# Kernel tuning notes

Measured on AMD Instinct MI355X. Metric: run time of the kernel, lower is better.

Reference implementation:

```python
import jax, jax.numpy as jnp
import numpy as np

B, T, C, H, E, MIN_E = 4, 2048, 1024, 128, 16, 2
IS_CAUSAL = False


def setup_inputs() -> dict:
    key = jax.random.key(0)
    ks = jax.random.split(key, 6)
    lim_qkv = float(np.sqrt(6.0 / (C + H)))
    inp = {
        "hidden_states": jax.random.normal(ks[0], (B, T, C), jnp.float32),
        "sim_matrix": jax.random.normal(ks[1], (C, E), jnp.float32),
        "gates": jnp.zeros((E,), jnp.float32),
        "q_proj": jax.random.uniform(ks[2], (E, C, H), jnp.float32, -lim_qkv, lim_qkv),
        "k_proj": jax.random.uniform(ks[3], (E, C, H), jnp.float32, -lim_qkv, lim_qkv),
        "v_proj": jax.random.uniform(ks[4], (E, C, H), jnp.float32, -lim_qkv, lim_qkv),
        "o_proj": jax.random.uniform(ks[5], (E, H, C), jnp.float32, -lim_qkv, lim_qkv),
    }
    return inp


def _forward(hidden_states, sim_matrix, gates, q_proj, k_proj, v_proj, o_proj):
    b, t, c = hidden_states.shape
    n = b * t
    x = hidden_states.reshape(n, c)

    # ---- gating (faithful to _gating_logic) ----
    xn = x / jnp.maximum(jnp.linalg.norm(x, axis=-1, keepdims=True), 1e-12)
    sn = sim_matrix / jnp.maximum(jnp.linalg.norm(sim_matrix, axis=0, keepdims=True), 1e-12)
    logits = xn @ sn - jax.nn.sigmoid(gates)          # [n, E]
    gated = jax.nn.relu(logits)
    # STE: forward = (gated > 0), backward = identity
    hard = (gated > 0).astype(gated.dtype)
    mask = gated + jax.lax.stop_gradient(hard - gated)
    inactive = (jnp.sum(hard, axis=1) == 0)
    # fallback: top-MIN_E logits for tokens with no active expert
    _, fb_idx = jax.lax.top_k(logits, MIN_E)
    fb = jnp.zeros((n, logits.shape[1]), gated.dtype).at[
        jnp.arange(n)[:, None], fb_idx].set(1.0)
    put = jax.lax.stop_gradient(inactive[:, None].astype(gated.dtype) * fb)
    mask = mask * (1.0 - put) + put                   # index_put semantics
    masked = jnp.where(mask > 0, gated, -jnp.inf)
    w = jax.nn.softmax(masked, axis=-1)               # routing weights [n, E]

    # ---- MoE dispatch/combine (dense-equivalent: w is exactly 0 where mask==0) ----
    def moe_proj(p):  # p: [E, C, H] -> [n, H]
        y = jnp.einsum('nc,ech->neh', x, p)
        return jnp.einsum('ne,neh->nh', w, y)

    q = moe_proj(q_proj).reshape(b, t, -1)
    k = moe_proj(k_proj).reshape(b, t, -1)
    v = moe_proj(v_proj).reshape(b, t, -1)

    # single-head SDPA, default scale 1/sqrt(head_dim)
    h = q.shape[-1]
    scores = jnp.einsum('bth,bsh->bts', q, k) / jnp.sqrt(jnp.asarray(h, q.dtype))
    if IS_CAUSAL and t > 1:
        causal = jnp.tril(jnp.ones((t, t), bool))
        scores = jnp.where(causal[None], scores, -jnp.inf)
    attn = jax.nn.softmax(scores, axis=-1)
    o = jnp.einsum('bts,bsh->bth', attn, v).reshape(n, h)

    # output MoE combine
    z = jnp.einsum('ne,nh->enh', w, o)                # [E, n, H]
    out = jnp.einsum('enh,ehc->nc', z, o_proj)
    return out.reshape(b, t, c)


def reference(hidden_states, sim_matrix, gates, q_proj, k_proj, v_proj, o_proj):
    return _forward(hidden_states, sim_matrix, gates, q_proj, k_proj, v_proj, o_proj)
```

## Files before the change

kernel.cpp:

```cpp
#include <hip/hip_runtime.h>
#include <hip/hip_bf16.h>
#include <math.h>

#define NBATCH 4
#define NT     2048
#define NC     1024
#define NH     128
#define NE     16
#define NTOK   (NBATCH * NT)
#define CAP    18432
#define NT2_MAX 152

typedef __bf16 bf16x8 __attribute__((ext_vector_type(8)));
typedef __bf16 bf16x4 __attribute__((ext_vector_type(4)));
typedef float  f32x4  __attribute__((ext_vector_type(4)));

__device__ __forceinline__ __bf16 f2bf(float f) { return (__bf16)f; }

#define BARRIER() __builtin_amdgcn_s_barrier()
#define SFENCE()  __builtin_amdgcn_sched_barrier(0)
#define VMWAIT(n) asm volatile("s_waitcnt vmcnt(" #n ")" ::: "memory")
#define LGKMWAIT0() asm volatile("s_waitcnt lgkmcnt(0)" ::: "memory")

__device__ __forceinline__ void gl_lds16(const void* g, void* l) {
  __builtin_amdgcn_global_load_lds((const __attribute__((address_space(1))) void*)g,
                                   (__attribute__((address_space(3))) void*)l, 16, 0, 0);
}

__device__ __forceinline__ const __bf16* swz_src(const __bf16* row0, size_t stride,
                                                 int tid, int i) {
  int lin = (tid + 256 * i) * 16;
  int r = lin >> 7, cb = lin & 127;
  return row0 + (size_t)r * stride + ((cb ^ ((r & 7) << 4)) >> 1);
}

__global__ void k_transpose_all(const float* __restrict__ qp, const float* __restrict__ kp,
                                const float* __restrict__ vp, const float* __restrict__ op,
                                __bf16* __restrict__ pqt, __bf16* __restrict__ pkt,
                                __bf16* __restrict__ pvt, __bf16* __restrict__ pot,
                                const float* __restrict__ sim, const float* __restrict__ gates,
                                double* __restrict__ snorm, double* __restrict__ sig,
                                int* __restrict__ ctrl) {
  __shared__ float tile[32][33];
  __shared__ double red[16][17];
  int z = blockIdx.y;
  int tid = threadIdx.x;
  if (z == 64) {
    if (blockIdx.x != 0) return;
    if (tid < 128) ctrl[tid] = 0;
    int e = tid & 15, chunk = tid >> 4;
    double a = 0.0;
#pragma unroll 4
    for (int j = 0; j < 64; j++) {
      double v = (double)sim[(chunk * 64 + j) * NE + e];
      a += v * v;
    }
    red[chunk][e] = a;
    __syncthreads();
    if (tid < 16) {
      double s = 0.0;
      for (int k = 0; k < 16; k++) s += red[k][tid];
      snorm[tid] = fmax(sqrt(s), 1e-12);
      sig[tid] = 1.0 / (1.0 + exp(-(double)gates[tid]));
    }
    return;
  }
  const float* in;
  __bf16* out;
  int R, Cd, g, r0, c0;
  if (z < 48) {
    int which = z >> 4; g = z & 15; R = 1024; Cd = 128;
    in = which == 0 ? qp : (which == 1 ? kp : vp);
    out = which == 0 ? pqt : (which == 1 ? pkt : pvt);
    r0 = (blockIdx.x >> 2) * 32; c0 = (blockIdx.x & 3) * 32;
  } else {
    g = z - 48; R = 128; Cd = 1024;
    in = op; out = pot;
    r0 = (blockIdx.x & 3) * 32; c0 = (blockIdx.x >> 2) * 32;
  }
  int tx = tid & 31, ty0 = tid >> 5;
  const float* src = in + (size_t)g * R * Cd;
  __bf16* dst = out + (size_t)g * R * Cd;
#pragma unroll
  for (int ty = ty0; ty < 32; ty += 8)
    tile[ty][tx] = src[(size_t)(r0 + ty) * Cd + (c0 + tx)];
  __syncthreads();
#pragma unroll
  for (int ty = ty0; ty < 32; ty += 8)
    dst[(size_t)(c0 + ty) * R + (r0 + tx)] = f2bf(tile[tx][ty]);
}

__global__ __launch_bounds__(256, 2) void k_gating3(const float* __restrict__ x,
                                                    const float* __restrict__ sim,
                                                    const double* __restrict__ snorm,
                                                    const double* __restrict__ sig,
                                                    float* __restrict__ w_all,
                                                    int* __restrict__ counts,
                                                    __bf16* __restrict__ xbf) {
  __shared__ union {
    struct {
      float xs_[16][66];
      float ss_[16][66];
    } s;
    double red[8][32][2][17];
  } u;
  __shared__ float w_lds[16][16];
  __shared__ int cnt_lds[16];
  int tid = threadIdx.x;
  if (tid < 16) cnt_lds[tid] = 0;
  int cg = tid & 31, tkg = tid >> 5;
  int tok0 = blockIdx.x * 16;

  double acc[2][17];
#pragma unroll
  for (int t = 0; t < 2; t++)
#pragma unroll
    for (int i = 0; i < 17; i++) acc[t][i] = 0.0;

  int xr0 = tid >> 4, xc4 = (tid & 15) * 4;
  int sr = tid >> 2, se4 = (tid & 3) * 4;

  float4 xa, sv;
  auto ldchunk = [&](int c0) {
    xa = *(const float4*)(x + (size_t)(tok0 + xr0) * NC + c0 + xc4);
    sv = *(const float4*)(sim + (size_t)(c0 + sr) * NE + se4);
  };
  auto stchunk = [&]() {
    *(float4*)&u.s.xs_[xr0][xc4] = xa;
    u.s.ss_[se4 + 0][sr] = sv.x;
    u.s.ss_[se4 + 1][sr] = sv.y;
    u.s.ss_[se4 + 2][sr] = sv.z;
    u.s.ss_[se4 + 3][sr] = sv.w;
  };
  auto stxbf = [&](int c0) {
    bf16x4 a;
    a[0]=f2bf(xa.x); a[1]=f2bf(xa.y); a[2]=f2bf(xa.z); a[3]=f2bf(xa.w);
    *(bf16x4*)(xbf + (size_t)(tok0 + xr0) * NC + c0 + xc4) = a;
  };

  ldchunk(0);
  for (int ch = 0; ch < 16; ch++) {
    stchunk();
    stxbf(ch * 64);
    __syncthreads();
    if (ch < 15) ldchunk((ch + 1) * 64);
    double xd[2][2];
#pragma unroll
    for (int t = 0; t < 2; t++) {
      float2 xv = *(const float2*)&u.s.xs_[tkg * 2 + t][cg * 2];
      xd[t][0] = (double)xv.x;
      xd[t][1] = (double)xv.y;
      acc[t][16] += xd[t][0] * xd[t][0] + xd[t][1] * xd[t][1];
    }
#pragma unroll
    for (int e = 0; e < 16; e++) {
      float2 sv2 = *(const float2*)&u.s.ss_[e][cg * 2];
      double s0 = (double)sv2.x, s1 = (double)sv2.y;
#pragma unroll
      for (int t = 0; t < 2; t++)
        acc[t][e] += xd[t][0] * s0 + xd[t][1] * s1;
    }
    __syncthreads();
  }

#pragma unroll
  for (int t = 0; t < 2; t++)
#pragma unroll
    for (int i = 0; i < 17; i++)
      u.red[tkg][cg][t][i] = acc[t][i];
  __syncthreads();

  if (tid < 16) {
    double dots[17];
    for (int i = 0; i < 17; i++) {
      double s = 0.0;
      for (int c = 0; c < 32; c++) s += u.red[tid >> 1][c][tid & 1][i];
      dots[i] = s;
    }
    double xn = fmax(sqrt(dots[16]), 1e-12);
    double logits[NE];
    unsigned act = 0;
    int cnt = 0;
    for (int ee = 0; ee < NE; ee++) {
      logits[ee] = dots[ee] / (xn * snorm[ee]) - sig[ee];
      if (logits[ee] > 0.0) { act |= 1u << ee; cnt++; }
    }
    if (cnt == 0) {
      int i1 = 0; double b1 = logits[0];
      for (int ee = 1; ee < NE; ee++) if (logits[ee] > b1) { b1 = logits[ee]; i1 = ee; }
      int i2 = -1; double b2 = -1e300;
      for (int ee = 0; ee < NE; ee++) if (ee != i1 && logits[ee] > b2) { b2 = logits[ee]; i2 = ee; }
      act = (1u << i1) | (1u << i2);
    }
    double m = -1e300;
    for (int ee = 0; ee < NE; ee++) if ((act >> ee) & 1) m = fmax(m, fmax(logits[ee], 0.0));
    double s = 0.0, wvv[NE];
    for (int ee = 0; ee < NE; ee++) {
      if ((act >> ee) & 1) { wvv[ee] = exp(fmax(logits[ee], 0.0) - m); s += wvv[ee]; }
      else wvv[ee] = 0.0;
    }
    for (int ee = 0; ee < NE; ee++) {
      if ((act >> ee) & 1) {
        w_lds[tid][ee] = (float)(wvv[ee] / s);
        atomicAdd(&cnt_lds[ee], 1);
      } else w_lds[tid][ee] = 0.0f;
    }
  }
  __syncthreads();
  w_all[(size_t)(tok0 + (tid >> 4)) * NE + (tid & 15)] = w_lds[tid >> 4][tid & 15];
  if (tid < 16 && cnt_lds[tid] > 0) atomicAdd(&counts[tid], cnt_lds[tid]);
}

__global__ void k_scan(const int* __restrict__ counts, int* __restrict__ offsets,
                       int2* __restrict__ tile_desc, int* __restrict__ n_tiles) {
  if (threadIdx.x == 0 && blockIdx.x == 0) {
    int off = 0, nt = 0;
    for (int e = 0; e < NE; e++) {
      offsets[e] = off;
      int c = counts[e];
      int tiles = (c + 127) >> 7;
      for (int t = 0; t < tiles; t++) {
        int s0 = off + t * 128;
        if (s0 < CAP && nt < NT2_MAX) { tile_desc[nt].x = e; tile_desc[nt].y = s0; nt++; }
      }
      off += c;
    }
    offsets[NE] = off;
    *n_tiles = nt;
  }
}

__global__ void k_assign(const float* __restrict__ w_all, const int* __restrict__ offsets,
                         int* __restrict__ cursors, int* __restrict__ slot_token,
                         float* __restrict__ slot_w, int* __restrict__ tok_slots,
                         int* __restrict__ tok_cnt) {
  int n = blockIdx.x * 256 + threadIdx.x;
  if (n >= NTOK) return;
  int j = 0;
  for (int e = 0; e < NE; e++) {
    float w = w_all[(size_t)n * NE + e];
    if (w > 0.0f) {
      int p = atomicAdd(&cursors[e], 1);
      int s = offsets[e] + p;
      slot_token[s] = n;
      slot_w[s] = w;
      tok_slots[n * 16 + j] = s;
      j++;
    }
  }
  tok_cnt[n] = j;
}

__device__ __forceinline__ void mfma_block(const __bf16* As, const __bf16* Bs,
                                           int lane, int wrow, f32x4 acc[8]) {
  const char* Ab = (const char*)As;
  const char* Bb = (const char*)Bs;
  int arow = wrow + (lane & 15);
  int rb = lane & 15;
#pragma unroll
  for (int ks = 0; ks < 2; ks++) {
    int kb = ks * 64 + (lane >> 4) * 16;
    bf16x8 af = *(const bf16x8*)(Ab + arow * 128 + (kb ^ ((arow & 7) << 4)));
#pragma unroll
    for (int nt = 0; nt < 8; nt++) {
      int brow = nt * 16 + rb;
      bf16x8 bv = *(const bf16x8*)(Bb + brow * 128 + (kb ^ ((brow & 7) << 4)));
      acc[nt] = __builtin_amdgcn_mfma_f32_16x16x32_bf16(af, bv, acc[nt], 0, 0, 0);
    }
  }
}

__device__ __forceinline__ void mfma_block128(const __bf16* As, const __bf16* Bs,
                                              int lane, int wrow2, f32x4 acc[2][8]) {
  const char* Ab = (const char*)As;
  const char* Bb = (const char*)Bs;
  int rb = lane & 15;
#pragma unroll
  for (int ks = 0; ks < 2; ks++) {
    int kb = ks * 64 + (lane >> 4) * 16;
    int ar = wrow2 + rb;
    int sw = kb ^ ((ar & 7) << 4);
    bf16x8 af0 = *(const bf16x8*)(Ab + ar * 128 + sw);
    bf16x8 af1 = *(const bf16x8*)(Ab + (ar + 16) * 128 + sw);
#pragma unroll
    for (int nt = 0; nt < 8; nt++) {
      int brow = nt * 16 + rb;
      bf16x8 bv = *(const bf16x8*)(Bb + brow * 128 + (kb ^ ((brow & 7) << 4)));
      acc[0][nt] = __builtin_amdgcn_mfma_f32_16x16x32_bf16(af0, bv, acc[0][nt], 0, 0, 0);
      acc[1][nt] = __builtin_amdgcn_mfma_f32_16x16x32_bf16(af1, bv, acc[1][nt], 0, 0, 0);
    }
  }
}

__device__ __forceinline__ void mfma_regA(bf16x8 af0, bf16x8 af1, const __bf16* Bs,
                                          int lane, f32x4 acc[8]) {
  const char* Bb = (const char*)Bs;
  int rb = lane & 15;
#pragma unroll
  for (int ks = 0; ks < 2; ks++) {
    int kb = ks * 64 + (lane >> 4) * 16;
    bf16x8 af = ks ? af1 : af0;
#pragma unroll
    for (int nt = 0; nt < 8; nt++) {
      int brow = nt * 16 + rb;
      bf16x8 bv = *(const bf16x8*)(Bb + brow * 128 + (kb ^ ((brow & 7) << 4)));
      acc[nt] = __builtin_amdgcn_mfma_f32_16x16x32_bf16(af, bv, acc[nt], 0, 0, 0);
    }
  }
}

__global__ __launch_bounds__(256) void k_moe_qkv2(
    const __bf16* __restrict__ xbf, const int* __restrict__ slot_token,
    const __bf16* __restrict__ pq, const __bf16* __restrict__ pk, const __bf16* __restrict__ pv,
    const int* __restrict__ offsets, const int2* __restrict__ tile_desc,
    const int* __restrict__ n_tiles,
    __bf16* __restrict__ yq, __bf16* __restrict__ yk, __bf16* __restrict__ yv) {
  int id = blockIdx.x;
  int w = (id & 7) * (3 * NT2_MAX / 8) + (id >> 3);
  int ti = w / 3, p = w % 3;
  if (ti >= *n_tiles) return;
  int2 td = tile_desc[ti];
  int e = td.x, s0 = td.y;
  int seg_end = offsets[e + 1]; if (seg_end > CAP) seg_end = CAP;
  const __bf16* Bt;
  __bf16* Yd;
  if (p == 0)      { Bt = pq; Yd = yq; }
  else if (p == 1) { Bt = pk; Yd = yk; }
  else             { Bt = pv; Yd = yv; }
  Bt += (size_t)e * NH * NC;

  __shared__ __bf16 As[2][128 * 64];
  __shared__ __bf16 Bs[2][128 * 64];
  int tid = threadIdx.x, lane = tid & 63, wid = tid >> 6, wrow2 = wid * 32;
  const __bf16* asrc[4];
  const __bf16* bsrc[4];
#pragma unroll
  for (int i = 0; i < 4; i++) {
    int lin = (tid + 256 * i) * 16;
    int r = lin >> 7, cb = lin & 127;
    int tok = slot_token[s0 + r] & (NTOK - 1);
    asrc[i] = xbf + (size_t)tok * NC + ((cb ^ ((r & 7) << 4)) >> 1);
  }
#pragma unroll
  for (int i = 0; i < 4; i++) bsrc[i] = swz_src(Bt, NC, tid, i);
  auto stage = [&](int buf, int k0) {
#pragma unroll
    for (int i = 0; i < 4; i++)
      gl_lds16(asrc[i] + k0, (char*)As[buf] + tid * 16 + i * 4096);
#pragma unroll
    for (int i = 0; i < 4; i++)
      gl_lds16(bsrc[i] + k0, (char*)Bs[buf] + tid * 16 + i * 4096);
  };

  f32x4 acc[2][8];
#pragma unroll
  for (int rf = 0; rf < 2; rf++)
#pragma unroll
    for (int i = 0; i < 8; i++) { f32x4 z = {0.f, 0.f, 0.f, 0.f}; acc[rf][i] = z; }

  stage(0, 0);
  stage(1, 64);
  VMWAIT(8); BARRIER(); SFENCE();
  int cur = 0;
  for (int t = 0; t <= 13; t++) {
    __builtin_amdgcn_s_setprio(1);
    mfma_block128(As[cur], Bs[cur], lane, wrow2, acc);
    __builtin_amdgcn_s_setprio(0);
    SFENCE();
    BARRIER();
    stage(cur, (t + 2) * 64);
    VMWAIT(8); BARRIER(); SFENCE();
    cur ^= 1;
  }
  __builtin_amdgcn_s_setprio(1);
  mfma_block128(As[cur], Bs[cur], lane, wrow2, acc);
  __builtin_amdgcn_s_setprio(0);
  SFENCE();
  VMWAIT(0); BARRIER(); SFENCE();
  __builtin_amdgcn_s_setprio(1);
  mfma_block128(As[cur ^ 1], Bs[cur ^ 1], lane, wrow2, acc);
  __builtin_amdgcn_s_setprio(0);

  int col = lane & 15, quad = lane >> 4;
#pragma unroll
  for (int rf = 0; rf < 2; rf++)
#pragma unroll
    for (int r = 0; r < 4; r++) {
      int s = s0 + wrow2 + rf * 16 + quad * 4 + r;
      if (s < seg_end) {
#pragma unroll
        for (int nt = 0; nt < 8; nt++)
          Yd[(size_t)s * NH + nt * 16 + col] = f2bf(acc[rf][nt][r]);
      }
    }
}

__global__ __launch_bounds__(256) void k_combine_qkv(
    const __bf16* __restrict__ yq, const __bf16* __restrict__ yk, const __bf16* __restrict__ yv,
    const int* __restrict__ tok_slots, const int* __restrict__ tok_cnt,
    const float* __restrict__ slot_w,
    __bf16* __restrict__ qb, __bf16* __restrict__ kb, __bf16* __restrict__ vt) {
  __shared__ __bf16 vtile[128][34];
  int tid = threadIdx.x;
  int tok0 = blockIdx.x * 32;
  int tt = tok0 + (tid >> 3);
  int h0 = (tid & 7) * 16;
  const __bf16* Y = blockIdx.y == 0 ? yq : (blockIdx.y == 1 ? yk : yv);
  int cnt = tok_cnt[tt];
  float acc[16];
#pragma unroll
  for (int i = 0; i < 16; i++) acc[i] = 0.f;
  for (int j = 0; j < cnt; j++) {
    int s = tok_slots[tt * 16 + j];
    if (s < CAP) {
      float w = slot_w[s];
      bf16x8 v0 = *(const bf16x8*)(Y + (size_t)s * NH + h0);
      bf16x8 v1 = *(const bf16x8*)(Y + (size_t)s * NH + h0 + 8);
#pragma unroll
      for (int i = 0; i < 8; i++) { acc[i] += w * (float)v0[i]; acc[8 + i] += w * (float)v1[i]; }
    }
  }
  if (blockIdx.y == 2) {
#pragma unroll
    for (int i = 0; i < 16; i++) vtile[h0 + i][tid >> 3] = f2bf(acc[i]);
    __syncthreads();
    int h = tid >> 1, tp = (tid & 1) * 16;
    int b = tok0 >> 11, trow = tok0 & 2047;
    __bf16* dst = vt + ((size_t)b * NH + h) * NT + trow + tp;
    bf16x8 o0, o1;
#pragma unroll
    for (int i = 0; i < 8; i++) { o0[i] = vtile[h][tp + i]; o1[i] = vtile[h][tp + 8 + i]; }
    *(bf16x8*)dst = o0;
    *(bf16x8*)(dst + 8) = o1;
  } else {
    float sc = blockIdx.y == 0 ? 0.12751744458115337f : 1.0f;
    __bf16* D = blockIdx.y == 0 ? qb : kb;
    bf16x8 o0, o1;
#pragma unroll
    for (int i = 0; i < 8; i++) { o0[i] = f2bf(acc[i] * sc); o1[i] = f2bf(acc[8 + i] * sc); }
    __bf16* d = D + (size_t)tt * NH + h0;
    *(bf16x8*)d = o0;
    *(bf16x8*)(d + 8) = o1;
  }
}

__global__ __launch_bounds__(256) void k_flash(const __bf16* __restrict__ q,
                                               const __bf16* __restrict__ k,
                                               const __bf16* __restrict__ vt,
                                               float* __restrict__ opart,
                                               float2* __restrict__ ml) {
  int id = blockIdx.x;
  int w = (id & 7) * 64 + (id >> 3);
  int b = w >> 7;
  int rem = w & 127;
  int spl = rem >> 5;
  int t0 = (rem & 31) * 64;
  const __bf16* qb = q + (size_t)b * NT * NH;
  const __bf16* kb = k + (size_t)b * NT * NH;
  const __bf16* vtb = vt + (size_t)b * NH * NT;

  __shared__ __bf16 Ks[2][128 * 64];
  __shared__ __bf16 Vs[2][128 * 64];
  __shared__ __bf16 Ps[2][64 * 64];
  int tid = threadIdx.x, lane = tid & 63, wid = tid >> 6, wrow = wid * 16;
  int colq = lane & 15, quad = lane >> 4;

  bf16x8 qf[4];
  {
    const __bf16* qr = qb + (size_t)(t0 + wrow + colq) * NH + quad * 8;
#pragma unroll
    for (int kk = 0; kk < 4; kk++) qf[kk] = *(const bf16x8*)(qr + kk * 32);
  }
  asm volatile("" :: "v"(qf[0]), "v"(qf[1]), "v"(qf[2]), "v"(qf[3]));
  SFENCE();

  auto stage_K = [&](int s0) {
#pragma unroll
    for (int c = 0; c < 2; c++)
#pragma unroll
      for (int i = 0; i < 4; i++)
        gl_lds16(swz_src(kb + (size_t)s0 * NH + c * 64, NH, tid, i),
                 (char*)Ks[c] + wid * 1024 + i * 4096);
  };
  auto stage_V = [&](int s0) {
#pragma unroll
    for (int c = 0; c < 2; c++)
#pragma unroll
      for (int i = 0; i < 4; i++)
        gl_lds16(swz_src(vtb + s0 + c * 64, NT, tid, i),
                 (char*)Vs[c] + wid * 1024 + i * 4096);
  };

  f32x4 oacc[8];
#pragma unroll
  for (int i = 0; i < 8; i++) { f32x4 z = {0.f, 0.f, 0.f, 0.f}; oacc[i] = z; }
  float mr[4], lr[4];
#pragma unroll
  for (int r = 0; r < 4; r++) { mr[r] = -1e30f; lr[r] = 0.f; }

  const int sbase = spl * 512;
  stage_K(sbase);
  stage_V(sbase);
  VMWAIT(8); BARRIER(); SFENCE();

  for (int t = 0; t < 4; t++) {
    f32x4 sacc[8];
#pragma unroll
    for (int i = 0; i < 8; i++) { f32x4 z = {0.f, 0.f, 0.f, 0.f}; sacc[i] = z; }
    __builtin_amdgcn_s_setprio(1);
    mfma_regA(qf[0], qf[1], Ks[0], lane, sacc);
    mfma_regA(qf[2], qf[3], Ks[1], lane, sacc);
    __builtin_amdgcn_s_setprio(0);
    SFENCE();
    BARRIER();
    if (t < 3) stage_K(sbase + (t + 1) * 128);

    float tm[4];
#pragma unroll
    for (int r = 0; r < 4; r++) {
      float v = sacc[0][r];
#pragma unroll
      for (int nt = 1; nt < 8; nt++) v = fmaxf(v, sacc[nt][r]);
      tm[r] = v;
    }
#pragma unroll
    for (int off = 1; off < 16; off <<= 1)
#pragma unroll
      for (int r = 0; r < 4; r++) tm[r] = fmaxf(tm[r], __shfl_xor(tm[r], off));
    float alpha[4], rs[4];
#pragma unroll
    for (int r = 0; r < 4; r++) {
      float mn = fmaxf(mr[r], tm[r]);
      alpha[r] = exp2f(mr[r] - mn);
      mr[r] = mn;
      rs[r] = 0.f;
    }
#pragma unroll
    for (int nt = 0; nt < 8; nt++) {
      char* pc = (char*)Ps[nt >> 2];
      int colb = ((nt & 3) * 16 + colq) * 2;
#pragma unroll
      for (int r = 0; r < 4; r++) {
        int row = wrow + quad * 4 + r;
        float p = exp2f(sacc[nt][r] - mr[r]);
        rs[r] += p;
        *(__bf16*)(pc + row * 128 + (colb ^ ((row & 7) << 4))) = f2bf(p);
      }
    }
#pragma unroll
    for (int off = 1; off < 16; off <<= 1)
#pragma unroll
      for (int r = 0; r < 4; r++) rs[r] += __shfl_xor(rs[r], off);
#pragma unroll
    for (int r = 0; r < 4; r++) lr[r] = alpha[r] * lr[r] + rs[r];
#pragma unroll
    for (int nt = 0; nt < 8; nt++)
#pragma unroll
      for (int r = 0; r < 4; r++) oacc[nt][r] *= alpha[r];

    LGKMWAIT0();
    if (t < 3) { VMWAIT(8); } else { VMWAIT(0); }
    BARRIER(); SFENCE();

    __builtin_amdgcn_s_setprio(1);
    mfma_block(Ps[0], Vs[0], lane, wrow, oacc);
    mfma_block(Ps[1], Vs[1], lane, wrow, oacc);
    __builtin_amdgcn_s_setprio(0);
    SFENCE();
    BARRIER();
    if (t < 3) {
      stage_V(sbase + (t + 1) * 128);
      VMWAIT(8); BARRIER(); SFENCE();
    }
  }

  size_t base = (size_t)(b * 4 + spl) * NT + t0;
#pragma unroll
  for (int r = 0; r < 4; r++) {
    size_t row = base + wrow + quad * 4 + r;
#pragma unroll
    for (int nt = 0; nt < 8; nt++)
      opart[row * NH + nt * 16 + colq] = oacc[nt][r];
  }
  if (colq == 0) {
#pragma unroll
    for (int r = 0; r < 4; r++) {
      float2 v; v.x = mr[r]; v.y = lr[r];
      ml[base + wrow + quad * 4 + r] = v;
    }
  }
}

__global__ __launch_bounds__(256) void k_gather_o(const float* __restrict__ opart,
                                                  const float2* __restrict__ ml,
                                                  const int* __restrict__ slot_token,
                                                  const int* __restrict__ offsets,
                                                  __bf16* __restrict__ og) {
  int slot = blockIdx.x * 2 + (threadIdx.x >> 7);
  int h = threadIdx.x & 127;
  int total = offsets[NE]; if (total > CAP) total = CAP;
  if (slot >= total) return;
  int n = slot_token[slot];
  int b = n >> 11, trow = n & 2047;
  size_t rb = (size_t)b * 4 * NT + trow;
  float2 m0 = ml[rb], m1 = ml[rb + NT], m2 = ml[rb + 2 * NT], m3 = ml[rb + 3 * NT];
  float M = fmaxf(fmaxf(m0.x, m1.x), fmaxf(m2.x, m3.x));
  float e0 = exp2f(m0.x - M), e1 = exp2f(m1.x - M), e2 = exp2f(m2.x - M), e3 = exp2f(m3.x - M);
  float den = m0.y * e0 + m1.y * e1 + m2.y * e2 + m3.y * e3;
  float num = opart[rb * NH + h] * e0 + opart[(rb + NT) * NH + h] * e1 +
              opart[(rb + 2 * NT) * NH + h] * e2 + opart[(rb + 3 * NT) * NH + h] * e3;
  og[(size_t)slot * NH + h] = f2bf(num / den);
}

__global__ __launch_bounds__(256) void k_out2(
    const __bf16* __restrict__ og, const __bf16* __restrict__ pot,
    const int* __restrict__ offsets, const int2* __restrict__ tile_desc,
    const int* __restrict__ n_tiles, __bf16* __restrict__ zy) {
  int id = blockIdx.x;
  int w = (id & 7) * (4 * NT2_MAX / 8) + (id >> 3);
  int ti = w >> 2, p = w & 3;
  if (ti >= *n_tiles) return;
  int2 td = tile_desc[ti];
  int e = td.x, s0 = td.y;
  int seg_end = offsets[e + 1]; if (seg_end > CAP) seg_end = CAP;
  int nc0 = p * 256;
  const __bf16* Bt = pot + (size_t)e * NC * NH;

  __shared__ __bf16 As[2][128 * 64];
  __shared__ __bf16 Bs[2][128 * 64];
  int tid = threadIdx.x, lane = tid & 63, wid = tid >> 6, wrow2 = wid * 32;
  const __bf16* asrc[4];
  const __bf16* bsrc[4];
#pragma unroll
  for (int i = 0; i < 4; i++) asrc[i] = swz_src(og + (size_t)s0 * NH, NH, tid, i);
#pragma unroll
  for (int i = 0; i < 4; i++) bsrc[i] = swz_src(Bt + (size_t)nc0 * NH, NH, tid, i);
  auto stageA = [&](int buf, int k0) {
#pragma unroll
    for (int i = 0; i < 4; i++)
      gl_lds16(asrc[i] + k0, (char*)As[buf] + tid * 16 + i * 4096);
  };
  auto stageB = [&](int buf, int k0, int noff) {
#pragma unroll
    for (int i = 0; i < 4; i++)
      gl_lds16(bsrc[i] + (size_t)noff * NH + k0, (char*)Bs[buf] + tid * 16 + i * 4096);
  };
  f32x4 acc[2][8];
  int col = lane & 15, quad = lane >> 4;
  auto store_acc = [&](int nco) {
#pragma unroll
    for (int rf = 0; rf < 2; rf++)
#pragma unroll
      for (int r = 0; r < 4; r++) {
        int s = s0 + wrow2 + rf * 16 + quad * 4 + r;
        if (s < seg_end) {
#pragma unroll
          for (int nt = 0; nt < 8; nt++)
            zy[(size_t)s * NC + nco + nt * 16 + col] = f2bf(acc[rf][nt][r]);
        }
      }
  };

#pragma unroll
  for (int rf = 0; rf < 2; rf++)
#pragma unroll
    for (int i = 0; i < 8; i++) { f32x4 z = {0.f, 0.f, 0.f, 0.f}; acc[rf][i] = z; }

  stageA(0, 0); stageB(0, 0, 0);
  stageA(1, 64); stageB(1, 64, 0);
  VMWAIT(8); BARRIER(); SFENCE();
  __builtin_amdgcn_s_setprio(1);
  mfma_block128(As[0], Bs[0], lane, wrow2, acc);
  __builtin_amdgcn_s_setprio(0);
  SFENCE();
  VMWAIT(0); BARRIER(); SFENCE();
  __builtin_amdgcn_s_setprio(1);
  mfma_block128(As[1], Bs[1], lane, wrow2, acc);
  __builtin_amdgcn_s_setprio(0);
  SFENCE();
  store_acc(nc0);
  BARRIER();
  stageB(0, 0, 128); stageB(1, 64, 128);
#pragma unroll
  for (int rf = 0; rf < 2; rf++)
#pragma unroll
    for (int i = 0; i < 8; i++) { f32x4 z = {0.f, 0.f, 0.f, 0.f}; acc[rf][i] = z; }
  VMWAIT(0); BARRIER(); SFENCE();
  __builtin_amdgcn_s_setprio(1);
  mfma_block128(As[0], Bs[0], lane, wrow2, acc);
  mfma_block128(As[1], Bs[1], lane, wrow2, acc);
  __builtin_amdgcn_s_setprio(0);
  store_acc(nc0 + 128);
}

__global__ __launch_bounds__(256) void k_combine_out(
    const __bf16* __restrict__ zy, const int* __restrict__ tok_slots,
    const int* __restrict__ tok_cnt, const float* __restrict__ slot_w,
    float* __restrict__ out) {
  int token = blockIdx.x;
  int c = threadIdx.x * 4;
  int cnt = tok_cnt[token];
  float a0 = 0.f, a1 = 0.f, a2 = 0.f, a3 = 0.f;
  for (int j = 0; j < cnt; j++) {
    int s = tok_slots[token * 16 + j];
    if (s < CAP) {
      float w = slot_w[s];
      bf16x4 z = *(const bf16x4*)&zy[(size_t)s * NC + c];
      a0 += w * (float)z[0];
      a1 += w * (float)z[1];
      a2 += w * (float)z[2];
      a3 += w * (float)z[3];
    }
  }
  float4 o = {a0, a1, a2, a3};
  *(float4*)&out[(size_t)token * NC + c] = o;
}

extern "C" void kernel_launch(void* const* d_in, const int* in_sizes, int n_in,
                              void* d_out, int out_size, void* d_ws, size_t ws_size,
                              hipStream_t stream) {
  const float* hs    = (const float*)d_in[0];
  const float* sim   = (const float*)d_in[1];
  const float* gates = (const float*)d_in[2];
  const float* qp    = (const float*)d_in[3];
  const float* kp    = (const float*)d_in[4];
  const float* vp    = (const float*)d_in[5];
  const float* op    = (const float*)d_in[6];
  float* out = (float*)d_out;
  char* ws = (char*)d_ws;

  const size_t M = 1048576;
  __bf16* PQT = (__bf16*)(ws + 0 * M);
  __bf16* PKT = (__bf16*)(ws + 4 * M);
  __bf16* PVT = (__bf16*)(ws + 8 * M);
  __bf16* POT = (__bf16*)(ws + 12 * M);
  __bf16* Qb  = (__bf16*)(ws + 16 * M);
  __bf16* Kb  = (__bf16*)(ws + 18 * M);
  __bf16* VT  = (__bf16*)(ws + 22 * M);
  float*  WALL = (float*)(ws + 28 * M);
  int*    STOK = (int*)(ws + 28 * M + 524288);
  float*  SW   = (float*)(ws + 28 * M + 1048576);
  int*    TSL  = (int*)(ws + 28 * M + 1572864);
  int*    TCN  = (int*)(ws + 28 * M + 2097152);
  double* SNORM = (double*)(ws + 28 * M + 2129920);
  double* SIG   = SNORM + 16;
  int* CNT = (int*)(ws + 28 * M + 2130432);
  int* OFF = CNT + 16;
  int* CUR = CNT + 40;
  int* NTL = CNT + 60;
  int2* DESC = (int2*)(ws + 28 * M + 2131456);
  __bf16* XBF = (__bf16*)(ws + 32 * M);
  __bf16* YQ = (__bf16*)(ws + 72 * M);
  __bf16* YK = (__bf16*)(ws + 77 * M);
  __bf16* YV = (__bf16*)(ws + 82 * M);
  float*  OP2 = (float*)(ws + 32 * M);
  float2* MLB = (float2*)(ws + 50 * M);
  __bf16* OG = (__bf16*)(ws + 52 * M);
  __bf16* ZY = (__bf16*)(ws + 60 * M);

  k_transpose_all<<<dim3(128, 65), 256, 0, stream>>>(qp, kp, vp, op, PQT, PKT, PVT, POT,
                                                     sim, gates, SNORM, SIG, CNT);
  k_gating3<<<NTOK / 16, 256, 0, stream>>>(hs, sim, SNORM, SIG, WALL, CNT, XBF);
  k_scan<<<1, 64, 0, stream>>>(CNT, OFF, DESC, NTL);
  k_assign<<<NTOK / 256, 256, 0, stream>>>(WALL, OFF, CUR, STOK, SW, TSL, TCN);
  k_moe_qkv2<<<3 * NT2_MAX, 256, 0, stream>>>(XBF, STOK, PQT, PKT, PVT, OFF, DESC, NTL, YQ, YK, YV);
  k_combine_qkv<<<dim3(NTOK / 32, 3), 256, 0, stream>>>(YQ, YK, YV, TSL, TCN, SW, Qb, Kb, VT);
  k_flash<<<512, 256, 0, stream>>>(Qb, Kb, VT, OP2, MLB);
  k_gather_o<<<CAP / 2, 256, 0, stream>>>(OP2, MLB, STOK, OFF, OG);
  k_out2<<<4 * NT2_MAX, 256, 0, stream>>>(OG, POT, OFF, DESC, NTL, ZY);
  k_combine_out<<<NTOK, 256, 0, stream>>>(ZY, TSL, TCN, SW, out);
}
```

Before: 273.5 us.

## Fuse weight transpose and gating into one front kernel; per-block counts; wave-aggregated atomics

Merges the weight transpose/convert kernel and the gating kernel into a single launch. Each gating block now computes the sim-matrix column norms redundantly instead of reading a separately computed result, and writes its per-expert counts to a buffer. The scan kernel reduces those counts and resets the cursors, which removes the global count atomics and the dependency between the two front kernels. The assign kernel uses wave ballot and popcount so that one atomic is issued per wave per expert. The cost is redundant norm work in every gating block and a larger union in shared memory.

```diff
diff --git a/kernel.cpp b/kernel.cpp
--- a/kernel.cpp
+++ b/kernel.cpp
@@ -34,37 +34,156 @@
   return row0 + (size_t)r * stride + ((cb ^ ((r & 7) << 4)) >> 1);
 }
 
-__global__ void k_transpose_all(const float* __restrict__ qp, const float* __restrict__ kp,
-                                const float* __restrict__ vp, const float* __restrict__ op,
-                                __bf16* __restrict__ pqt, __bf16* __restrict__ pkt,
-                                __bf16* __restrict__ pvt, __bf16* __restrict__ pot,
-                                const float* __restrict__ sim, const float* __restrict__ gates,
-                                double* __restrict__ snorm, double* __restrict__ sig,
-                                int* __restrict__ ctrl) {
-  __shared__ float tile[32][33];
-  __shared__ double red[16][17];
-  int z = blockIdx.y;
+__global__ __launch_bounds__(256, 2) void k_front(
+    const float* __restrict__ x, const float* __restrict__ sim,
+    const float* __restrict__ gates,
+    const float* __restrict__ qp, const float* __restrict__ kp,
+    const float* __restrict__ vp, const float* __restrict__ op,
+    __bf16* __restrict__ pqt, __bf16* __restrict__ pkt,
+    __bf16* __restrict__ pvt, __bf16* __restrict__ pot,
+    float* __restrict__ w_all, int* __restrict__ cntb, __bf16* __restrict__ xbf) {
+  __shared__ union {
+    struct {
+      float xs_[16][66];
+      float ss_[16][66];
+    } s;
+    double red[8][32][2][17];
+    float ttile[32][33];
+  } u;
+  __shared__ double snred[32][16];
+  __shared__ double snorm_lds[16];
+  __shared__ double sig_lds[16];
+  __shared__ float w_lds[16][16];
+  __shared__ int cnt_lds[16];
+  int id = blockIdx.x;
   int tid = threadIdx.x;
-  if (z == 64) {
-    if (blockIdx.x != 0) return;
-    if (tid < 128) ctrl[tid] = 0;
-    int e = tid & 15, chunk = tid >> 4;
-    double a = 0.0;
-#pragma unroll 4
-    for (int j = 0; j < 64; j++) {
-      double v = (double)sim[(chunk * 64 + j) * NE + e];
-      a += v * v;
-    }
-    red[chunk][e] = a;
+
+  if (id < 512) {
+    if (tid < 16) {
+      cnt_lds[tid] = 0;
+      sig_lds[tid] = 1.0 / (1.0 + exp(-(double)gates[tid]));
+    }
+    int cg = tid & 31, tkg = tid >> 5;
+    int tok0 = id * 16;
+
+    double acc[2][17];
+#pragma unroll
+    for (int t = 0; t < 2; t++)
+#pragma unroll
+      for (int i = 0; i < 17; i++) acc[t][i] = 0.0;
+    double sn[16];
+#pragma unroll
+    for (int i = 0; i < 16; i++) sn[i] = 0.0;
+    bool dosn = tid < 64;
+
+    int xr0 = tid >> 4, xc4 = (tid & 15) * 4;
+    int sr = tid >> 2, se4 = (tid & 3) * 4;
+
+    float4 xa, sv;
+    auto ldchunk = [&](int c0) {
+      xa = *(const float4*)(x + (size_t)(tok0 + xr0) * NC + c0 + xc4);
+      sv = *(const float4*)(sim + (size_t)(c0 + sr) * NE + se4);
+    };
+    auto stchunk = [&]() {
+      *(float4*)&u.s.xs_[xr0][xc4] = xa;
+      u.s.ss_[se4 + 0][sr] = sv.x;
+      u.s.ss_[se4 + 1][sr] = sv.y;
+      u.s.ss_[se4 + 2][sr] = sv.z;
+      u.s.ss_[se4 + 3][sr] = sv.w;
+    };
+    auto stxbf = [&](int c0) {
+      bf16x4 a;
+      a[0]=f2bf(xa.x); a[1]=f2bf(xa.y); a[2]=f2bf(xa.z); a[3]=f2bf(xa.w);
+      *(bf16x4*)(xbf + (size_t)(tok0 + xr0) * NC + c0 + xc4) = a;
+    };
+
+    ldchunk(0);
+    for (int ch = 0; ch < 16; ch++) {
+      stchunk();
+      stxbf(ch * 64);
+      __syncthreads();
+      if (ch < 15) ldchunk((ch + 1) * 64);
+      double xd[2][2];
+#pragma unroll
+      for (int t = 0; t < 2; t++) {
+        float2 xv = *(const float2*)&u.s.xs_[tkg * 2 + t][cg * 2];
+        xd[t][0] = (double)xv.x;
+        xd[t][1] = (double)xv.y;
+        acc[t][16] += xd[t][0] * xd[t][0] + xd[t][1] * xd[t][1];
+      }
+#pragma unroll
+      for (int e = 0; e < 16; e++) {
+        float2 sv2 = *(const float2*)&u.s.ss_[e][cg * 2];
+        double s0 = (double)sv2.x, s1 = (double)sv2.y;
+#pragma unroll
+        for (int t = 0; t < 2; t++)
+          acc[t][e] += xd[t][0] * s0 + xd[t][1] * s1;
+        if (dosn) sn[e] += s0 * s0 + s1 * s1;
+      }
+      __syncthreads();
+    }
+
+#pragma unroll
+    for (int t = 0; t < 2; t++)
+#pragma unroll
+      for (int i = 0; i < 17; i++)
+        u.red[tkg][cg][t][i] = acc[t][i];
+    if (tid < 32)
+#pragma unroll
+      for (int e = 0; e < 16; e++) snred[tid][e] = sn[e];
     __syncthreads();
+
     if (tid < 16) {
       double s = 0.0;
-      for (int k = 0; k < 16; k++) s += red[k][tid];
-      snorm[tid] = fmax(sqrt(s), 1e-12);
-      sig[tid] = 1.0 / (1.0 + exp(-(double)gates[tid]));
-    }
+      for (int c = 0; c < 32; c++) s += snred[c][tid];
+      snorm_lds[tid] = fmax(sqrt(s), 1e-12);
+    }
+    __syncthreads();
+
+    if (tid < 16) {
+      double dots[17];
+      for (int i = 0; i < 17; i++) {
+        double s = 0.0;
+        for (int c = 0; c < 32; c++) s += u.red[tid >> 1][c][tid & 1][i];
+        dots[i] = s;
+      }
+      double xn = fmax(sqrt(dots[16]), 1e-12);
+      double logits[NE];
+      unsigned act = 0;
+      int cnt = 0;
+      for (int ee = 0; ee < NE; ee++) {
+        logits[ee] = dots[ee] / (xn * snorm_lds[ee]) - sig_lds[ee];
+        if (logits[ee] > 0.0) { act |= 1u << ee; cnt++; }
+      }
+      if (cnt == 0) {
+        int i1 = 0; double b1 = logits[0];
+        for (int ee = 1; ee < NE; ee++) if (logits[ee] > b1) { b1 = logits[ee]; i1 = ee; }
+        int i2 = -1; double b2 = -1e300;
+        for (int ee = 0; ee < NE; ee++) if (ee != i1 && logits[ee] > b2) { b2 = logits[ee]; i2 = ee; }
+        act = (1u << i1) | (1u << i2);
+      }
+      double m = -1e300;
+      for (int ee = 0; ee < NE; ee++) if ((act >> ee) & 1) m = fmax(m, fmax(logits[ee], 0.0));
+      double s = 0.0, wvv[NE];
+      for (int ee = 0; ee < NE; ee++) {
+        if ((act >> ee) & 1) { wvv[ee] = exp(fmax(logits[ee], 0.0) - m); s += wvv[ee]; }
+        else wvv[ee] = 0.0;
+      }
+      for (int ee = 0; ee < NE; ee++) {
+        if ((act >> ee) & 1) {
+          w_lds[tid][ee] = (float)(wvv[ee] / s);
+          atomicAdd(&cnt_lds[ee], 1);
+        } else w_lds[tid][ee] = 0.0f;
+      }
+    }
+    __syncthreads();
+    w_all[(size_t)(tok0 + (tid >> 4)) * NE + (tid & 15)] = w_lds[tid >> 4][tid & 15];
+    if (tid < 16) cntb[id * 16 + tid] = cnt_lds[tid];
     return;
   }
+
+  int t2 = id - 512;
+  int z = t2 >> 7, xb = t2 & 127;
   const float* in;
   __bf16* out;
   int R, Cd, g, r0, c0;
@@ -72,156 +191,45 @@
     int which = z >> 4; g = z & 15; R = 1024; Cd = 128;
     in = which == 0 ? qp : (which == 1 ? kp : vp);
     out = which == 0 ? pqt : (which == 1 ? pkt : pvt);
-    r0 = (blockIdx.x >> 2) * 32; c0 = (blockIdx.x & 3) * 32;
+    r0 = (xb >> 2) * 32; c0 = (xb & 3) * 32;
   } else {
     g = z - 48; R = 128; Cd = 1024;
     in = op; out = pot;
-    r0 = (blockIdx.x & 3) * 32; c0 = (blockIdx.x >> 2) * 32;
+    r0 = (xb & 3) * 32; c0 = (xb >> 2) * 32;
   }
   int tx = tid & 31, ty0 = tid >> 5;
   const float* src = in + (size_t)g * R * Cd;
   __bf16* dst = out + (size_t)g * R * Cd;
 #pragma unroll
   for (int ty = ty0; ty < 32; ty += 8)
-    tile[ty][tx] = src[(size_t)(r0 + ty) * Cd + (c0 + tx)];
+    u.ttile[ty][tx] = src[(size_t)(r0 + ty) * Cd + (c0 + tx)];
   __syncthreads();
 #pragma unroll
   for (int ty = ty0; ty < 32; ty += 8)
-    dst[(size_t)(c0 + ty) * R + (r0 + tx)] = f2bf(tile[tx][ty]);
-}
-
-__global__ __launch_bounds__(256, 2) void k_gating3(const float* __restrict__ x,
-                                                    const float* __restrict__ sim,
-                                                    const double* __restrict__ snorm,
-                                                    const double* __restrict__ sig,
-                                                    float* __restrict__ w_all,
-                                                    int* __restrict__ counts,
-                                                    __bf16* __restrict__ xbf) {
-  __shared__ union {
-    struct {
-      float xs_[16][66];
-      float ss_[16][66];
-    } s;
-    double red[8][32][2][17];
-  } u;
-  __shared__ float w_lds[16][16];
-  __shared__ int cnt_lds[16];
+    dst[(size_t)(c0 + ty) * R + (r0 + tx)] = f2bf(u.ttile[tx][ty]);
+}
+
+__global__ void k_scan(const int* __restrict__ cntb, int* __restrict__ offsets,
+                       int2* __restrict__ tile_desc, int* __restrict__ n_tiles,
+                       int* __restrict__ cursors) {
+  __shared__ int part[16][17];
   int tid = threadIdx.x;
-  if (tid < 16) cnt_lds[tid] = 0;
-  int cg = tid & 31, tkg = tid >> 5;
-  int tok0 = blockIdx.x * 16;
-
-  double acc[2][17];
-#pragma unroll
-  for (int t = 0; t < 2; t++)
-#pragma unroll
-    for (int i = 0; i < 17; i++) acc[t][i] = 0.0;
-
-  int xr0 = tid >> 4, xc4 = (tid & 15) * 4;
-  int sr = tid >> 2, se4 = (tid & 3) * 4;
-
-  float4 xa, sv;
-  auto ldchunk = [&](int c0) {
-    xa = *(const float4*)(x + (size_t)(tok0 + xr0) * NC + c0 + xc4);
-    sv = *(const float4*)(sim + (size_t)(c0 + sr) * NE + se4);
-  };
-  auto stchunk = [&]() {
-    *(float4*)&u.s.xs_[xr0][xc4] = xa;
-    u.s.ss_[se4 + 0][sr] = sv.x;
-    u.s.ss_[se4 + 1][sr] = sv.y;
-    u.s.ss_[se4 + 2][sr] = sv.z;
-    u.s.ss_[se4 + 3][sr] = sv.w;
-  };
-  auto stxbf = [&](int c0) {
-    bf16x4 a;
-    a[0]=f2bf(xa.x); a[1]=f2bf(xa.y); a[2]=f2bf(xa.z); a[3]=f2bf(xa.w);
-    *(bf16x4*)(xbf + (size_t)(tok0 + xr0) * NC + c0 + xc4) = a;
-  };
-
-  ldchunk(0);
-  for (int ch = 0; ch < 16; ch++) {
-    stchunk();
-    stxbf(ch * 64);
-    __syncthreads();
-    if (ch < 15) ldchunk((ch + 1) * 64);
-    double xd[2][2];
-#pragma unroll
-    for (int t = 0; t < 2; t++) {
-      float2 xv = *(const float2*)&u.s.xs_[tkg * 2 + t][cg * 2];
-      xd[t][0] = (double)xv.x;
-      xd[t][1] = (double)xv.y;
-      acc[t][16] += xd[t][0] * xd[t][0] + xd[t][1] * xd[t][1];
-    }
-#pragma unroll
-    for (int e = 0; e < 16; e++) {
-      float2 sv2 = *(const float2*)&u.s.ss_[e][cg * 2];
-      double s0 = (double)sv2.x, s1 = (double)sv2.y;
-#pragma unroll
-      for (int t = 0; t < 2; t++)
-        acc[t][e] += xd[t][0] * s0 + xd[t][1] * s1;
-    }
-    __syncthreads();
-  }
-
-#pragma unroll
-  for (int t = 0; t < 2; t++)
-#pragma unroll
-    for (int i = 0; i < 17; i++)
-      u.red[tkg][cg][t][i] = acc[t][i];
+  int e = tid & 15, pp = tid >> 4;
+  int s = 0;
+  for (int b = pp; b < 512; b += 16) s += cntb[b * 16 + e];
+  part[pp][e] = s;
   __syncthreads();
-
-  if (tid < 16) {
-    double dots[17];
-    for (int i = 0; i < 17; i++) {
-      double s = 0.0;
-      for (int c = 0; c < 32; c++) s += u.red[tid >> 1][c][tid & 1][i];
-      dots[i] = s;
-    }
-    double xn = fmax(sqrt(dots[16]), 1e-12);
-    double logits[NE];
-    unsigned act = 0;
-    int cnt = 0;
+  if (tid >= 16 && tid < 32) cursors[tid - 16] = 0;
+  if (tid == 0) {
+    int off = 0, nt = 0;
     for (int ee = 0; ee < NE; ee++) {
-      logits[ee] = dots[ee] / (xn * snorm[ee]) - sig[ee];
-      if (logits[ee] > 0.0) { act |= 1u << ee; cnt++; }
-    }
-    if (cnt == 0) {
-      int i1 = 0; double b1 = logits[0];
-      for (int ee = 1; ee < NE; ee++) if (logits[ee] > b1) { b1 = logits[ee]; i1 = ee; }
-      int i2 = -1; double b2 = -1e300;
-      for (int ee = 0; ee < NE; ee++) if (ee != i1 && logits[ee] > b2) { b2 = logits[ee]; i2 = ee; }
-      act = (1u << i1) | (1u << i2);
-    }
-    double m = -1e300;
-    for (int ee = 0; ee < NE; ee++) if ((act >> ee) & 1) m = fmax(m, fmax(logits[ee], 0.0));
-    double s = 0.0, wvv[NE];
-    for (int ee = 0; ee < NE; ee++) {
-      if ((act >> ee) & 1) { wvv[ee] = exp(fmax(logits[ee], 0.0) - m); s += wvv[ee]; }
-      else wvv[ee] = 0.0;
-    }
-    for (int ee = 0; ee < NE; ee++) {
-      if ((act >> ee) & 1) {
-        w_lds[tid][ee] = (float)(wvv[ee] / s);
-        atomicAdd(&cnt_lds[ee], 1);
-      } else w_lds[tid][ee] = 0.0f;
-    }
-  }
-  __syncthreads();
-  w_all[(size_t)(tok0 + (tid >> 4)) * NE + (tid & 15)] = w_lds[tid >> 4][tid & 15];
-  if (tid < 16 && cnt_lds[tid] > 0) atomicAdd(&counts[tid], cnt_lds[tid]);
-}
-
-__global__ void k_scan(const int* __restrict__ counts, int* __restrict__ offsets,
-                       int2* __restrict__ tile_desc, int* __restrict__ n_tiles) {
-  if (threadIdx.x == 0 && blockIdx.x == 0) {
-    int off = 0, nt = 0;
-    for (int e = 0; e < NE; e++) {
-      offsets[e] = off;
-      int c = counts[e];
+      int c = 0;
+      for (int p = 0; p < 16; p++) c += part[p][ee];
+      offsets[ee] = off;
       int tiles = (c + 127) >> 7;
       for (int t = 0; t < tiles; t++) {
         int s0 = off + t * 128;
-        if (s0 < CAP && nt < NT2_MAX) { tile_desc[nt].x = e; tile_desc[nt].y = s0; nt++; }
+        if (s0 < CAP && nt < NT2_MAX) { tile_desc[nt].x = ee; tile_desc[nt].y = s0; nt++; }
       }
       off += c;
     }
@@ -235,17 +243,25 @@
                          float* __restrict__ slot_w, int* __restrict__ tok_slots,
                          int* __restrict__ tok_cnt) {
   int n = blockIdx.x * 256 + threadIdx.x;
-  if (n >= NTOK) return;
+  int lane = threadIdx.x & 63;
   int j = 0;
   for (int e = 0; e < NE; e++) {
     float w = w_all[(size_t)n * NE + e];
-    if (w > 0.0f) {
-      int p = atomicAdd(&cursors[e], 1);
-      int s = offsets[e] + p;
-      slot_token[s] = n;
-      slot_w[s] = w;
-      tok_slots[n * 16 + j] = s;
-      j++;
+    bool a = w > 0.0f;
+    unsigned long long mask = __ballot(a);
+    if (mask) {
+      int leader = (int)__ffsll((long long)mask) - 1;
+      int base = 0;
+      if (lane == leader) base = atomicAdd(&cursors[e], (int)__popcll(mask));
+      base = __shfl(base, leader);
+      if (a) {
+        int pos = base + (int)__popcll(mask & ((1ULL << lane) - 1ULL));
+        int s = offsets[e] + pos;
+        slot_token[s] = n;
+        slot_w[s] = w;
+        tok_slots[n * 16 + j] = s;
+        j++;
+      }
     }
   }
   tok_cnt[n] = j;
@@ -737,13 +753,12 @@
   __bf16* Qb  = (__bf16*)(ws + 16 * M);
   __bf16* Kb  = (__bf16*)(ws + 18 * M);
   __bf16* VT  = (__bf16*)(ws + 22 * M);
+  int*    CNTB = (int*)(ws + 27 * M);
   float*  WALL = (float*)(ws + 28 * M);
   int*    STOK = (int*)(ws + 28 * M + 524288);
   float*  SW   = (float*)(ws + 28 * M + 1048576);
   int*    TSL  = (int*)(ws + 28 * M + 1572864);
   int*    TCN  = (int*)(ws + 28 * M + 2097152);
-  double* SNORM = (double*)(ws + 28 * M + 2129920);
-  double* SIG   = SNORM + 16;
   int* CNT = (int*)(ws + 28 * M + 2130432);
   int* OFF = CNT + 16;
   int* CUR = CNT + 40;
@@ -758,10 +773,9 @@
   __bf16* OG = (__bf16*)(ws + 52 * M);
   __bf16* ZY = (__bf16*)(ws + 60 * M);
 
-  k_transpose_all<<<dim3(128, 65), 256, 0, stream>>>(qp, kp, vp, op, PQT, PKT, PVT, POT,
-                                                     sim, gates, SNORM, SIG, CNT);
-  k_gating3<<<NTOK / 16, 256, 0, stream>>>(hs, sim, SNORM, SIG, WALL, CNT, XBF);
-  k_scan<<<1, 64, 0, stream>>>(CNT, OFF, DESC, NTL);
+  k_front<<<512 + 64 * 128, 256, 0, stream>>>(hs, sim, gates, qp, kp, vp, op,
+                                              PQT, PKT, PVT, POT, WALL, CNTB, XBF);
+  k_scan<<<1, 256, 0, stream>>>(CNTB, OFF, DESC, NTL, CUR);
   k_assign<<<NTOK / 256, 256, 0, stream>>>(WALL, OFF, CUR, STOK, SW, TSL, TCN);
   k_moe_qkv2<<<3 * NT2_MAX, 256, 0, stream>>>(XBF, STOK, PQT, PKT, PVT, OFF, DESC, NTL, YQ, YK, YV);
   k_combine_qkv<<<dim3(NTOK / 32, 3), 256, 0, stream>>>(YQ, YK, YV, TSL, TCN, SW, Qb, Kb, VT);
```

Measured after the change: 371.6 us. +35.9%, slower.
